# Performance work log

Measured on AMD Instinct MI355X. Metric: run time of the kernel, lower is better.

The kernel has to match this reference:

```python
import jax, jax.numpy as jnp
import numpy as np

HEADS = 8
HEAD_DIM = 64
EPS = 1e-5


def setup_inputs() -> dict:
    key = jax.random.key(0)
    k1, k2, k3 = jax.random.split(key, 3)
    dim, hidden = 512, HEADS * HEAD_DIM
    x = jax.random.normal(k1, (8, dim, 64, 64), dtype=jnp.float32)
    w_qkv = jax.random.normal(k2, (hidden * 3, dim), dtype=jnp.float32) * (dim ** -0.5)
    w_out = jax.random.normal(k3, (dim, hidden), dtype=jnp.float32) * (hidden ** -0.5)
    b_out = jnp.zeros((dim,), dtype=jnp.float32)
    g = jnp.ones((dim,), dtype=jnp.float32)
    return {"x": x, "w_qkv": w_qkv, "w_out": w_out, "b_out": b_out, "g": g}


def reference(x, w_qkv, w_out, b_out, g):
    b, c, h, w = x.shape
    n = h * w
    scale = HEAD_DIM ** -0.5
    xf = x.reshape(b, c, n)  # 1x1 conv == channel matmul
    qkv = jnp.einsum('oc,bcn->bon', w_qkv, xf)
    q, k, v = jnp.split(qkv, 3, axis=1)
    def to_heads(t):
        return t.reshape(b, HEADS, HEAD_DIM, n)
    q, k, v = to_heads(q), to_heads(k), to_heads(v)
    q = jax.nn.softmax(q, axis=-2) * scale   # softmax over head_dim
    k = jax.nn.softmax(k, axis=-1)           # softmax over tokens
    v = v / n
    # context: (B,H,d,d) = k (B,H,d,N) @ v^T (B,H,N,e)
    context = jnp.einsum('bhdn,bhen->bhde', k, v)
    # out: context^T (e,d) @ q (d,N) -> (B,H,e,N)
    out = jnp.einsum('bhde,bhdn->bhen', context, q)
    out = out.reshape(b, HEADS * HEAD_DIM, n)
    y = jnp.einsum('co,bon->bcn', w_out, out) + b_out[None, :, None]
    # channel LayerNorm (mean/var over dim=1, biased var, scale g only)
    mean = jnp.mean(y, axis=1, keepdims=True)
    var = jnp.var(y, axis=1, keepdims=True)
    y = (y - mean) * jax.lax.rsqrt(var + EPS) * g[None, :, None]
    return y.reshape(b, c, h, w)
```

## Files before the change

### kernel.cpp

```cpp
#include <hip/hip_runtime.h>
#include <math.h>

#define BB 8
#define NN 4096
#define CD 512
#define HH 8
#define DD 64
#define OC3 1536
#define NSPLIT 16

typedef _Float16 f16;
typedef _Float16 half8 __attribute__((ext_vector_type(8)));
typedef _Float16 half4v __attribute__((ext_vector_type(4)));
typedef float f32x4 __attribute__((ext_vector_type(4)));

__device__ __forceinline__ void gload_lds16(const void* g, void* l) {
    __builtin_amdgcn_global_load_lds(
        (const __attribute__((address_space(1))) unsigned int*)g,
        (__attribute__((address_space(3))) unsigned int*)l, 16, 0, 0);
}

__global__ __launch_bounds__(256) void split_w_kernel(
    const float* __restrict__ w, f16* __restrict__ wh, f16* __restrict__ wl)
{
    int idx = blockIdx.x * 256 + threadIdx.x;
    float4 v = ((const float4*)w)[idx];
    float a[4] = {v.x, v.y, v.z, v.w};
    half4v h, l;
    #pragma unroll
    for (int i = 0; i < 4; ++i) {
        float s = a[i] * 64.f;
        f16 hh = (f16)s;
        h[i] = hh;
        l[i] = (f16)(s - (float)hh);
    }
    *(half4v*)(&wh[(long)idx * 4]) = h;
    *(half4v*)(&wl[(long)idx * 4]) = l;
}

__global__ __launch_bounds__(256) void split_x_kernel(
    const float* __restrict__ x, f16* __restrict__ xth, f16* __restrict__ xtl)
{
    __shared__ float tile[64][65];
    int b = blockIdx.z;
    int n0 = blockIdx.x * 64, c0 = blockIdx.y * 64;
    const float* xb = x + ((long)b * CD + c0) * NN + n0;
    int t = threadIdx.x;
    int tr = t >> 6, tc = t & 63;
    #pragma unroll
    for (int i = 0; i < 16; ++i)
        tile[tr + i * 4][tc] = xb[(long)(tr + i * 4) * NN + tc];
    __syncthreads();

    int nl = t >> 3, ck = (t & 7) * 8;
    long obase = ((long)b * NN + n0) * CD + c0;
    #pragma unroll
    for (int p = 0; p < 2; ++p) {
        int n = nl + p * 32;
        half8 h, l;
        #pragma unroll
        for (int j = 0; j < 8; ++j) {
            float s = tile[ck + j][n] * 16.f;
            f16 hv = (f16)s;
            h[j] = hv;
            l[j] = (f16)(s - (float)hv);
        }
        *(half8*)(&xth[obase + (long)n * CD + ck]) = h;
        *(half8*)(&xtl[obase + (long)n * CD + ck]) = l;
    }
}

#define AR  16384
#define BUF 65536

#define STAGE(Lb, k0s)  do {                                                   \
    long kb_ = (long)(k0s) * 2;                                                \
    _Pragma("unroll")                                                          \
    for (int c_ = 0; c_ < 2; ++c_) {                                           \
        long rowoff_ = (long)(rb0 + c_ * 16) * 1024;                           \
        long ldsoff_ = (long)(rb0 + c_ * 16) * 64;                             \
        gload_lds16(gA_h + rowoff_ + kb_ + g_lane, (Lb) + 0 * AR + ldsoff_);   \
        gload_lds16(gA_l + rowoff_ + kb_ + g_lane, (Lb) + 1 * AR + ldsoff_);   \
        gload_lds16(gB_h + rowoff_ + kb_ + g_lane, (Lb) + 2 * AR + ldsoff_);   \
        gload_lds16(gB_l + rowoff_ + kb_ + g_lane, (Lb) + 3 * AR + ldsoff_);   \
    } } while (0)

__global__ __launch_bounds__(512, 2) void mfma_gemm_kernel(
    const f16* __restrict__ Ah, const f16* __restrict__ Al, long sA,
    const f16* __restrict__ Bh, const f16* __restrict__ Bl, long sB,
    float* __restrict__ Cp, long sC, int ldC,
    const float* __restrict__ bias, const float* __restrict__ inv_sc,
    float base_sc, int fuseqv)
{
    __shared__ f16 lds[2][4][256 * 32];
    int bz = blockIdx.z;
    int n0 = blockIdx.x * 256, m0 = blockIdx.y * 256;
    int t = threadIdx.x;
    int lane = t & 63, wid = t >> 6;
    int wy = wid >> 2, wx = wid & 3;

    int cl = (lane & 3) ^ ((lane >> 3) & 3);
    long g_lane = (long)(lane >> 2) * 1024 + (long)cl * 16;

    const char* gA_h = (const char*)(Ah + bz * sA) + (long)m0 * 1024;
    const char* gA_l = (const char*)(Al + bz * sA) + (long)m0 * 1024;
    const char* gB_h = (const char*)(Bh + bz * sB) + (long)n0 * 1024;
    const char* gB_l = (const char*)(Bl + bz * sB) + (long)n0 * 1024;

    char* L0 = (char*)&lds[0][0][0];
    int rb0 = wid * 32;

    int cp = (lane >> 4) ^ (((lane & 15) >> 1) & 3);
    long offA = (long)(wy * 128 + (lane & 15)) * 64 + (long)cp * 16;
    long offB = (long)(wx * 64 + (lane & 15)) * 64 + (long)cp * 16;

    f32x4 acc[8][4];
    #pragma unroll
    for (int i = 0; i < 8; ++i)
        #pragma unroll
        for (int j = 0; j < 4; ++j)
            acc[i][j] = (f32x4){0.f, 0.f, 0.f, 0.f};

    STAGE(L0, 0);
    asm volatile("s_waitcnt vmcnt(0)" ::: "memory");
    __syncthreads();

    for (int s = 0; s < 16; ++s) {
        char* Lc = L0 + ((s & 1) ? BUF : 0);
        if (s < 15) {
            char* Ln = L0 + (((s + 1) & 1) ? BUF : 0);
            STAGE(Ln, (s + 1) * 32);
        }

        half8 ah[8], al[8];
        #pragma unroll
        for (int i = 0; i < 8; ++i) {
            ah[i] = *(const half8*)(Lc + 0 * AR + offA + i * 1024);
            al[i] = *(const half8*)(Lc + 1 * AR + offA + i * 1024);
        }
        #pragma unroll
        for (int j = 0; j < 4; ++j) {
            half8 bh = *(const half8*)(Lc + 2 * AR + offB + j * 1024);
            half8 bl = *(const half8*)(Lc + 3 * AR + offB + j * 1024);
            #pragma unroll
            for (int i = 0; i < 8; ++i) {
                acc[i][j] = __builtin_amdgcn_mfma_f32_16x16x32_f16(ah[i], bh, acc[i][j], 0, 0, 0);
                acc[i][j] = __builtin_amdgcn_mfma_f32_16x16x32_f16(ah[i], bl, acc[i][j], 0, 0, 0);
                acc[i][j] = __builtin_amdgcn_mfma_f32_16x16x32_f16(al[i], bh, acc[i][j], 0, 0, 0);
            }
        }

        asm volatile("s_waitcnt vmcnt(0)" ::: "memory");
        __syncthreads();
    }

    int colb = n0 + wx * 64 + (lane & 15);
    int rowb = m0 + wy * 128 + ((lane >> 4) << 2);

    if (fuseqv && m0 < 512) {
        int h0 = (m0 >> 6) + wy * 2;
        f16* qh_b = (f16*)(Cp + (long)bz * sC);
        f16* ql_b = qh_b + (long)CD * NN;
        #pragma unroll
        for (int i = 0; i < 8; ++i)
            #pragma unroll
            for (int j = 0; j < 4; ++j)
                #pragma unroll
                for (int r = 0; r < 4; ++r)
                    acc[i][j][r] *= base_sc;
        #pragma unroll
        for (int j = 0; j < 4; ++j) {
            long nj = colb + j * 16;
            #pragma unroll
            for (int g = 0; g < 2; ++g) {
                float mx = -INFINITY;
                #pragma unroll
                for (int di = 0; di < 4; ++di)
                    #pragma unroll
                    for (int r = 0; r < 4; ++r)
                        mx = fmaxf(mx, acc[g * 4 + di][j][r]);
                mx = fmaxf(mx, __shfl_xor(mx, 16));
                mx = fmaxf(mx, __shfl_xor(mx, 32));
                float sum = 0.f;
                #pragma unroll
                for (int di = 0; di < 4; ++di)
                    #pragma unroll
                    for (int r = 0; r < 4; ++r) {
                        float e = expf(acc[g * 4 + di][j][r] - mx);
                        acc[g * 4 + di][j][r] = e;
                        sum += e;
                    }
                sum += __shfl_xor(sum, 16);
                sum += __shfl_xor(sum, 32);
                float rj = 32.f / sum;
                long off = nj * CD + (h0 + g) * 64 + ((lane >> 4) << 2);
                #pragma unroll
                for (int di = 0; di < 4; ++di) {
                    half4v hh, ll;
                    #pragma unroll
                    for (int r = 0; r < 4; ++r) {
                        float v = acc[g * 4 + di][j][r] * rj;
                        f16 hv = (f16)v;
                        hh[r] = hv;
                        ll[r] = (f16)(v - (float)hv);
                    }
                    *(half4v*)(qh_b + off + di * 16) = hh;
                    *(half4v*)(ql_b + off + di * 16) = ll;
                }
            }
        }
        return;
    }

    if (fuseqv && m0 >= 1024) {
        f16* vhp = (f16*)(Cp + (long)bz * sC + 2L * CD * NN);
        f16* vlp = vhp + (long)CD * NN;
        float vsc = base_sc * 16.f;
        #pragma unroll
        for (int i = 0; i < 8; ++i)
            #pragma unroll
            for (int j = 0; j < 4; ++j)
                #pragma unroll
                for (int r = 0; r < 4; ++r) {
                    long row = rowb + i * 16 + r - 1024;
                    float val = acc[i][j][r] * vsc;
                    f16 hv = (f16)val;
                    vhp[row * NN + colb + j * 16] = hv;
                    vlp[row * NN + colb + j * 16] = (f16)(val - (float)hv);
                }
        return;
    }

    float* outp = Cp + bz * sC;
    float mult = base_sc * (inv_sc ? inv_sc[bz] : 1.f);
    #pragma unroll
    for (int i = 0; i < 8; ++i)
        #pragma unroll
        for (int j = 0; j < 4; ++j)
            #pragma unroll
            for (int r = 0; r < 4; ++r) {
                int row = rowb + i * 16 + r;
                float bb = bias ? bias[row] : 0.f;
                outp[(long)row * ldC + colb + j * 16] = acc[i][j][r] * mult + bb;
            }
}

__global__ __launch_bounds__(256) void softmax_k_kernel(
    const float* __restrict__ qkv, f16* __restrict__ ksp)
{
    int row = blockIdx.x;
    int b = row >> 9;
    int hd = row & (CD - 1);
    const float* base = qkv + ((long)b * OC3 + CD + hd) * NN;
    f16* khb = ksp + (long)b * 2 * CD * NN + (long)hd * NN;
    f16* klb = khb + (long)CD * NN;
    int t = threadIdx.x;

    float v[16];
    #pragma unroll
    for (int i = 0; i < 16; ++i) v[i] = base[t + i * 256];

    __shared__ float red[256];
    float mx = -INFINITY;
    #pragma unroll
    for (int i = 0; i < 16; ++i) mx = fmaxf(mx, v[i]);
    red[t] = mx; __syncthreads();
    for (int off = 128; off > 0; off >>= 1) {
        if (t < off) red[t] = fmaxf(red[t], red[t + off]);
        __syncthreads();
    }
    mx = red[0]; __syncthreads();

    float s = 0.f;
    #pragma unroll
    for (int i = 0; i < 16; ++i) {
        v[i] = expf(v[i] - mx);
        s += v[i];
    }
    red[t] = s; __syncthreads();
    for (int off = 128; off > 0; off >>= 1) {
        if (t < off) red[t] += red[t + off];
        __syncthreads();
    }
    float inv = 4096.f / red[0];

    #pragma unroll
    for (int i = 0; i < 16; ++i) {
        float val = v[i] * inv;
        f16 hv = (f16)val;
        khb[t + i * 256] = hv;
        klb[t + i * 256] = (f16)(val - (float)hv);
    }
}

__global__ __launch_bounds__(256) void ctx_mfma_kernel(
    const f16* __restrict__ ksp, const float* __restrict__ qkv,
    float* __restrict__ ctxp)
{
    __shared__ f16 lds[4][64 * 32];
    int sp = blockIdx.x;
    int bh = blockIdx.y;
    int b = bh >> 3, h = bh & 7;
    int t = threadIdx.x, lane = t & 63, w = t >> 6;

    const char* khg = (const char*)(ksp + (long)b * 2 * CD * NN) + (long)h * 64 * (NN * 2);
    const char* klg = khg + (long)CD * NN * 2;
    const char* vhg = (const char*)(qkv + ((long)b * OC3 + 2L * CD) * NN) + (long)h * 64 * (NN * 2);
    const char* vlg = vhg + (long)CD * NN * 2;
    const char* gw = (w == 0) ? khg : (w == 1) ? klg : (w == 2) ? vhg : vlg;

    int cl = (lane & 3) ^ ((lane >> 3) & 3);
    char* larr = (char*)&lds[0][0] + w * 4096;
    char* L = (char*)&lds[0][0];
    int cp16 = ((lane >> 4) ^ (((lane & 15) >> 1) & 3)) * 16;
    int lr = lane & 15;

    f32x4 acc[4];
    #pragma unroll
    for (int i = 0; i < 4; ++i) acc[i] = (f32x4){0.f, 0.f, 0.f, 0.f};

    for (int ks = 0; ks < 8; ++ks) {
        long kbyte = ((long)sp * 256 + ks * 32) * 2;
        #pragma unroll
        for (int c = 0; c < 4; ++c)
            gload_lds16(gw + (long)(c * 16 + (lane >> 2)) * (NN * 2) + kbyte + (long)cl * 16,
                        larr + c * 1024 + lane * 16);
        asm volatile("s_waitcnt vmcnt(0)" ::: "memory");
        __syncthreads();

        half8 ah[4], al[4], bhf, blf;
        #pragma unroll
        for (int i = 0; i < 4; ++i) {
            ah[i] = *(const half8*)(L + 0 * 4096 + (i * 16 + lr) * 64 + cp16);
            al[i] = *(const half8*)(L + 1 * 4096 + (i * 16 + lr) * 64 + cp16);
        }
        bhf = *(const half8*)(L + 2 * 4096 + (w * 16 + lr) * 64 + cp16);
        blf = *(const half8*)(L + 3 * 4096 + (w * 16 + lr) * 64 + cp16);
        #pragma unroll
        for (int i = 0; i < 4; ++i) {
            acc[i] = __builtin_amdgcn_mfma_f32_16x16x32_f16(ah[i], bhf, acc[i], 0, 0, 0);
            acc[i] = __builtin_amdgcn_mfma_f32_16x16x32_f16(ah[i], blf, acc[i], 0, 0, 0);
            acc[i] = __builtin_amdgcn_mfma_f32_16x16x32_f16(al[i], bhf, acc[i], 0, 0, 0);
        }
        __syncthreads();
    }

    float* op = ctxp + ((long)bh * NSPLIT + sp) * 4096;
    #pragma unroll
    for (int i = 0; i < 4; ++i)
        #pragma unroll
        for (int r = 0; r < 4; ++r)
            op[(i * 16 + (lane >> 4) * 4 + r) * 64 + w * 16 + lr] = acc[i][r];
}

__global__ __launch_bounds__(256) void fold_wout_kernel(
    const float* __restrict__ w_out, const float* __restrict__ ctxp,
    float* __restrict__ Mf)
{
    __shared__ float cl[64][65];
    int bh = blockIdx.x;
    int b = bh >> 3, h = bh & 7;
    int t = threadIdx.x;
    const float* cp = ctxp + (long)bh * NSPLIT * 4096;
    #pragma unroll
    for (int i = 0; i < 16; ++i) {
        int de = t + i * 256;
        double s = 0.0;
        #pragma unroll
        for (int sp = 0; sp < NSPLIT; ++sp)
            s += (double)cp[(long)sp * 4096 + de];
        cl[de >> 6][de & 63] = (float)(s * (1.0 / 268435456.0));
    }
    __syncthreads();

    int d = t & 63, tc = t >> 6;
    for (int ci = 0; ci < 128; ++ci) {
        int c = tc * 128 + ci;
        const float* wr = w_out + (long)c * CD + h * DD;
        float s = 0.f;
        #pragma unroll
        for (int e = 0; e < 64; ++e) s += wr[e] * cl[d][e];
        Mf[((long)b * CD + c) * CD + h * DD + d] = s;
    }
}

__global__ __launch_bounds__(256) void max_m_part_kernel(
    const float* __restrict__ Mf, float* __restrict__ part)
{
    int blk = blockIdx.x;
    int b = blk >> 5, sub = blk & 31;
    const float4* p = (const float4*)(Mf + (long)b * CD * CD) + (long)sub * 2048;
    float mx = 0.f;
    for (int i = threadIdx.x; i < 2048; i += 256) {
        float4 v = p[i];
        mx = fmaxf(mx, fmaxf(fmaxf(fabsf(v.x), fabsf(v.y)),
                             fmaxf(fabsf(v.z), fabsf(v.w))));
    }
    __shared__ float red[256];
    red[threadIdx.x] = mx; __syncthreads();
    for (int off = 128; off > 0; off >>= 1) {
        if (threadIdx.x < off) red[threadIdx.x] = fmaxf(red[threadIdx.x], red[threadIdx.x + off]);
        __syncthreads();
    }
    if (threadIdx.x == 0) part[blk] = red[0];
}

__global__ __launch_bounds__(64) void max_m_final_kernel(
    const float* __restrict__ part, float* __restrict__ scl)
{
    int b = threadIdx.x;
    if (b < 8) {
        float m = 0.f;
        #pragma unroll
        for (int i = 0; i < 32; ++i) m = fmaxf(m, part[b * 32 + i]);
        int e = (m > 1e-30f) ? ilogbf(m) : 0;
        scl[b] = ldexpf(1.f, 10 - e);
        scl[8 + b] = ldexpf(1.f, e - 10);
    }
}

__global__ __launch_bounds__(256) void split_m_kernel(
    const float* __restrict__ Mf, const float* __restrict__ scl,
    f16* __restrict__ mh, f16* __restrict__ ml)
{
    int idx = blockIdx.x * 256 + threadIdx.x;
    float s = scl[idx >> 16];
    float4 v = ((const float4*)Mf)[idx];
    float a[4] = {v.x, v.y, v.z, v.w};
    half4v h, l;
    #pragma unroll
    for (int i = 0; i < 4; ++i) {
        float tval = a[i] * s;
        f16 hv = (f16)tval;
        h[i] = hv;
        l[i] = (f16)(tval - (float)hv);
    }
    *(half4v*)(&mh[(long)idx * 4]) = h;
    *(half4v*)(&ml[(long)idx * 4]) = l;
}

__global__ __launch_bounds__(256) void layernorm_kernel(
    const float* __restrict__ qkv, const float* __restrict__ g,
    float* __restrict__ out)
{
    int t = threadIdx.x;
    int tn = t & 31, cy = t >> 5;
    long col = (long)blockIdx.x * 32 + tn;
    int n = (int)(col & (NN - 1));
    int b = (int)(col >> 12);
    const float* base = qkv + (long)b * OC3 * NN + (long)CD * NN + n;

    float v[64];
    double s = 0.0, ss = 0.0;
    #pragma unroll
    for (int i = 0; i < 64; ++i) {
        v[i] = base[(long)(cy * 64 + i) * NN];
        s += (double)v[i];
        ss += (double)v[i] * (double)v[i];
    }

    __shared__ double rs[8][32], rss[8][32];
    rs[cy][tn] = s; rss[cy][tn] = ss;
    __syncthreads();
    __shared__ float mb[32], ib[32];
    if (cy == 0) {
        double S = 0.0, SS = 0.0;
        #pragma unroll
        for (int j = 0; j < 8; ++j) { S += rs[j][tn]; SS += rss[j][tn]; }
        double mean = S * (1.0 / CD);
        double var = SS * (1.0 / CD) - mean * mean;
        mb[tn] = (float)mean;
        ib[tn] = (float)(1.0 / sqrt(var + 1e-5));
    }
    __syncthreads();
    float m = mb[tn], iv = ib[tn];

    float* oc = out + (long)b * CD * NN + n;
    #pragma unroll
    for (int i = 0; i < 64; ++i)
        oc[(long)(cy * 64 + i) * NN] = (v[i] - m) * iv * g[cy * 64 + i];
}

extern "C" void kernel_launch(void* const* d_in, const int* in_sizes, int n_in,
                              void* d_out, int out_size, void* d_ws, size_t ws_size,
                              hipStream_t stream)
{
    const float* x     = (const float*)d_in[0];
    const float* w_qkv = (const float*)d_in[1];
    const float* w_out = (const float*)d_in[2];
    const float* b_out = (const float*)d_in[3];
    const float* g     = (const float*)d_in[4];
    float* out = (float*)d_out;

    float* ws   = (float*)d_ws;
    float* qkv  = ws;
    float* ctxp = qkv + (long)BB * OC3 * NN;
    f16*   mh   = (f16*)(ctxp + (long)BB * HH * NSPLIT * DD * DD);
    f16*   ml   = mh + (long)BB * CD * CD;
    f16*   wh   = (f16*)(ml + (long)BB * CD * CD);
    f16*   wl   = wh + (long)OC3 * CD;
    float* scl  = (float*)(wl + (long)OC3 * CD);
    float* part = scl + 16;

    f16* xth = (f16*)d_out;
    f16* xtl = xth + (long)BB * NN * CD;
    f16* ksp = (f16*)d_out;
    float* Mf = (float*)d_out;

    split_w_kernel<<<(OC3 * CD / 4) / 256, 256, 0, stream>>>(w_qkv, wh, wl);
    split_x_kernel<<<dim3(NN / 64, CD / 64, BB), 256, 0, stream>>>(x, xth, xtl);

    mfma_gemm_kernel<<<dim3(NN / 256, OC3 / 256, BB), 512, 0, stream>>>(
        wh, wl, 0L, xth, xtl, (long)NN * CD,
        qkv, (long)OC3 * NN, NN, nullptr, nullptr, 1.0f / 1024.0f, 1);

    softmax_k_kernel<<<BB * CD, 256, 0, stream>>>(qkv, ksp);

    ctx_mfma_kernel<<<dim3(NSPLIT, BB * HH), 256, 0, stream>>>(ksp, qkv, ctxp);

    fold_wout_kernel<<<BB * HH, 256, 0, stream>>>(w_out, ctxp, Mf);
    max_m_part_kernel<<<256, 256, 0, stream>>>(Mf, part);
    max_m_final_kernel<<<1, 64, 0, stream>>>(part, scl);
    split_m_kernel<<<(BB * CD * CD / 4) / 256, 256, 0, stream>>>(Mf, scl, mh, ml);

    mfma_gemm_kernel<<<dim3(NN / 256, CD / 256, BB), 512, 0, stream>>>(
        mh, ml, (long)CD * CD,
        (const f16*)qkv, (const f16*)qkv + (long)CD * NN, (long)OC3 * NN * 2,
        qkv + (long)CD * NN, (long)OC3 * NN, NN, b_out, scl + 8, 1.0f / 256.0f,
        0);

    layernorm_kernel<<<(BB * NN) / 32, 256, 0, stream>>>(qkv, g, out);
}
```

Measured before the change: 423.4 us.

## Fuse K softmax into context MFMA kernel and add 128-tile output GEMM

The K softmax no longer writes a normalized f16 hi/lo copy of K. A row-stat kernel now stores only the per-row max and inverse sum. The context kernel loads raw fp32 K, applies exp and scale, and splits it into hi/lo halves in registers before the MFMAs, which removes a full write and re-read of K. The final output GEMM moves to a new 128x128-tile kernel with 256 threads, which launches more blocks for the small M=512 case. The cost is recomputing exp inside the context kernel and reading fp32 K at twice the byte width.

```diff
diff --git a/kernel.cpp b/kernel.cpp
--- a/kernel.cpp
+++ b/kernel.cpp
@@ -88,9 +88,7 @@
 __global__ __launch_bounds__(512, 2) void mfma_gemm_kernel(
     const f16* __restrict__ Ah, const f16* __restrict__ Al, long sA,
     const f16* __restrict__ Bh, const f16* __restrict__ Bl, long sB,
-    float* __restrict__ Cp, long sC, int ldC,
-    const float* __restrict__ bias, const float* __restrict__ inv_sc,
-    float base_sc, int fuseqv)
+    float* __restrict__ Cp, long sC, int ldC, float base_sc)
 {
     __shared__ f16 lds[2][4][256 * 32];
     int bz = blockIdx.z;
@@ -157,7 +155,7 @@
     int colb = n0 + wx * 64 + (lane & 15);
     int rowb = m0 + wy * 128 + ((lane >> 4) << 2);
 
-    if (fuseqv && m0 < 512) {
+    if (m0 < 512) {
         int h0 = (m0 >> 6) + wy * 2;
         f16* qh_b = (f16*)(Cp + (long)bz * sC);
         f16* ql_b = qh_b + (long)CD * NN;
@@ -212,7 +210,7 @@
         return;
     }
 
-    if (fuseqv && m0 >= 1024) {
+    if (m0 >= 1024) {
         f16* vhp = (f16*)(Cp + (long)bz * sC + 2L * CD * NN);
         f16* vlp = vhp + (long)CD * NN;
         float vsc = base_sc * 16.f;
@@ -232,9 +230,106 @@
     }
 
     float* outp = Cp + bz * sC;
+    #pragma unroll
+    for (int i = 0; i < 8; ++i)
+        #pragma unroll
+        for (int j = 0; j < 4; ++j)
+            #pragma unroll
+            for (int r = 0; r < 4; ++r) {
+                int row = rowb + i * 16 + r;
+                outp[(long)row * ldC + colb + j * 16] = acc[i][j][r] * base_sc;
+            }
+}
+
+#define AR2  8192
+#define BUF2 32768
+
+#define STAGE2(Lb, k0s)  do {                                                  \
+    long kb_ = (long)(k0s) * 2;                                                \
+    _Pragma("unroll")                                                          \
+    for (int c_ = 0; c_ < 2; ++c_) {                                           \
+        long rowoff_ = (long)(rb0 + c_ * 16) * 1024;                           \
+        long ldsoff_ = (long)(rb0 + c_ * 16) * 64;                             \
+        gload_lds16(gA_h + rowoff_ + kb_ + g_lane, (Lb) + 0 * AR2 + ldsoff_);  \
+        gload_lds16(gA_l + rowoff_ + kb_ + g_lane, (Lb) + 1 * AR2 + ldsoff_);  \
+        gload_lds16(gB_h + rowoff_ + kb_ + g_lane, (Lb) + 2 * AR2 + ldsoff_);  \
+        gload_lds16(gB_l + rowoff_ + kb_ + g_lane, (Lb) + 3 * AR2 + ldsoff_);  \
+    } } while (0)
+
+__global__ __launch_bounds__(256) void mfma_gemm128_kernel(
+    const f16* __restrict__ Ah, const f16* __restrict__ Al, long sA,
+    const f16* __restrict__ Bh, const f16* __restrict__ Bl, long sB,
+    float* __restrict__ Cp, long sC, int ldC,
+    const float* __restrict__ bias, const float* __restrict__ inv_sc,
+    float base_sc)
+{
+    __shared__ f16 lds[2][4][128 * 32];
+    int bz = blockIdx.z;
+    int n0 = blockIdx.x * 128, m0 = blockIdx.y * 128;
+    int t = threadIdx.x;
+    int lane = t & 63, wid = t >> 6;
+    int wy = wid >> 1, wx = wid & 1;
+
+    int cl = (lane & 3) ^ ((lane >> 3) & 3);
+    long g_lane = (long)(lane >> 2) * 1024 + (long)cl * 16;
+
+    const char* gA_h = (const char*)(Ah + bz * sA) + (long)m0 * 1024;
+    const char* gA_l = (const char*)(Al + bz * sA) + (long)m0 * 1024;
+    const char* gB_h = (const char*)(Bh + bz * sB) + (long)n0 * 1024;
+    const char* gB_l = (const char*)(Bl + bz * sB) + (long)n0 * 1024;
+
+    char* L0 = (char*)&lds[0][0][0];
+    int rb0 = wid * 32;
+
+    int cp = (lane >> 4) ^ (((lane & 15) >> 1) & 3);
+    long offA = (long)(wy * 64 + (lane & 15)) * 64 + (long)cp * 16;
+    long offB = (long)(wx * 64 + (lane & 15)) * 64 + (long)cp * 16;
+
+    f32x4 acc[4][4];
+    #pragma unroll
+    for (int i = 0; i < 4; ++i)
+        #pragma unroll
+        for (int j = 0; j < 4; ++j)
+            acc[i][j] = (f32x4){0.f, 0.f, 0.f, 0.f};
+
+    STAGE2(L0, 0);
+    asm volatile("s_waitcnt vmcnt(0)" ::: "memory");
+    __syncthreads();
+
+    for (int s = 0; s < 16; ++s) {
+        char* Lc = L0 + ((s & 1) ? BUF2 : 0);
+        if (s < 15) {
+            char* Ln = L0 + (((s + 1) & 1) ? BUF2 : 0);
+            STAGE2(Ln, (s + 1) * 32);
+        }
+
+        half8 ah[4], al[4], bh[4], bl[4];
+        #pragma unroll
+        for (int i = 0; i < 4; ++i) {
+            ah[i] = *(const half8*)(Lc + 0 * AR2 + offA + i * 1024);
+            al[i] = *(const half8*)(Lc + 1 * AR2 + offA + i * 1024);
+            bh[i] = *(const half8*)(Lc + 2 * AR2 + offB + i * 1024);
+            bl[i] = *(const half8*)(Lc + 3 * AR2 + offB + i * 1024);
+        }
+        #pragma unroll
+        for (int i = 0; i < 4; ++i)
+            #pragma unroll
+            for (int j = 0; j < 4; ++j) {
+                acc[i][j] = __builtin_amdgcn_mfma_f32_16x16x32_f16(ah[i], bh[j], acc[i][j], 0, 0, 0);
+                acc[i][j] = __builtin_amdgcn_mfma_f32_16x16x32_f16(ah[i], bl[j], acc[i][j], 0, 0, 0);
+                acc[i][j] = __builtin_amdgcn_mfma_f32_16x16x32_f16(al[i], bh[j], acc[i][j], 0, 0, 0);
+            }
+
+        asm volatile("s_waitcnt vmcnt(0)" ::: "memory");
+        __syncthreads();
+    }
+
+    int colb = n0 + wx * 64 + (lane & 15);
+    int rowb = m0 + wy * 64 + ((lane >> 4) << 2);
+    float* outp = Cp + bz * sC;
     float mult = base_sc * (inv_sc ? inv_sc[bz] : 1.f);
     #pragma unroll
-    for (int i = 0; i < 8; ++i)
+    for (int i = 0; i < 4; ++i)
         #pragma unroll
         for (int j = 0; j < 4; ++j)
             #pragma unroll
@@ -245,15 +340,14 @@
             }
 }
 
-__global__ __launch_bounds__(256) void softmax_k_kernel(
-    const float* __restrict__ qkv, f16* __restrict__ ksp)
+__global__ __launch_bounds__(256) void k_rowstat_kernel(
+    const float* __restrict__ qkv, float* __restrict__ statmx,
+    float* __restrict__ statinv)
 {
     int row = blockIdx.x;
     int b = row >> 9;
     int hd = row & (CD - 1);
     const float* base = qkv + ((long)b * OC3 + CD + hd) * NN;
-    f16* khb = ksp + (long)b * 2 * CD * NN + (long)hd * NN;
-    f16* klb = khb + (long)CD * NN;
     int t = threadIdx.x;
 
     float v[16];
@@ -282,60 +376,86 @@
         if (t < off) red[t] += red[t + off];
         __syncthreads();
     }
-    float inv = 4096.f / red[0];
-
-    #pragma unroll
-    for (int i = 0; i < 16; ++i) {
-        float val = v[i] * inv;
-        f16 hv = (f16)val;
-        khb[t + i * 256] = hv;
-        klb[t + i * 256] = (f16)(val - (float)hv);
+    if (t == 0) {
+        statmx[row] = mx;
+        statinv[row] = 4096.f / red[0];
     }
 }
 
 __global__ __launch_bounds__(256) void ctx_mfma_kernel(
-    const f16* __restrict__ ksp, const float* __restrict__ qkv,
-    float* __restrict__ ctxp)
-{
-    __shared__ f16 lds[4][64 * 32];
+    const float* __restrict__ qkv, const float* __restrict__ statmx,
+    const float* __restrict__ statinv, float* __restrict__ ctxp)
+{
+    __shared__ char lds[16384];
     int sp = blockIdx.x;
     int bh = blockIdx.y;
     int b = bh >> 3, h = bh & 7;
     int t = threadIdx.x, lane = t & 63, w = t >> 6;
 
-    const char* khg = (const char*)(ksp + (long)b * 2 * CD * NN) + (long)h * 64 * (NN * 2);
-    const char* klg = khg + (long)CD * NN * 2;
+    const char* kg = (const char*)(qkv + ((long)b * OC3 + CD + (long)h * 64) * NN);
     const char* vhg = (const char*)(qkv + ((long)b * OC3 + 2L * CD) * NN) + (long)h * 64 * (NN * 2);
     const char* vlg = vhg + (long)CD * NN * 2;
-    const char* gw = (w == 0) ? khg : (w == 1) ? klg : (w == 2) ? vhg : vlg;
+
+    int lr = lane & 15, hi = lane >> 4;
+    float mx[4], inv[4];
+    #pragma unroll
+    for (int i = 0; i < 4; ++i) {
+        int ridx = b * CD + h * 64 + i * 16 + lr;
+        mx[i] = statmx[ridx];
+        inv[i] = statinv[ridx];
+    }
 
     int cl = (lane & 3) ^ ((lane >> 3) & 3);
-    char* larr = (char*)&lds[0][0] + w * 4096;
-    char* L = (char*)&lds[0][0];
-    int cp16 = ((lane >> 4) ^ (((lane & 15) >> 1) & 3)) * 16;
-    int lr = lane & 15;
+    int cp16 = (hi ^ ((lr >> 1) & 3)) * 16;
+
+    int ksrow = (lane >> 3);
+    int ksc = lane & 7;
 
     f32x4 acc[4];
     #pragma unroll
     for (int i = 0; i < 4; ++i) acc[i] = (f32x4){0.f, 0.f, 0.f, 0.f};
 
+    int s7 = lr & 7;
+
     for (int ks = 0; ks < 8; ++ks) {
-        long kbyte = ((long)sp * 256 + ks * 32) * 2;
-        #pragma unroll
-        for (int c = 0; c < 4; ++c)
-            gload_lds16(gw + (long)(c * 16 + (lane >> 2)) * (NN * 2) + kbyte + (long)cl * 16,
-                        larr + c * 1024 + lane * 16);
+        int n0 = sp * 256 + ks * 32;
+        if (w < 2) {
+            #pragma unroll
+            for (int it2 = 0; it2 < 4; ++it2) {
+                int it = w * 4 + it2;
+                int r = it * 8 + ksrow;
+                gload_lds16(kg + (long)r * (NN * 4) + (long)n0 * 4 + ((ksc ^ (r & 7)) << 4),
+                            lds + it * 1024 + lane * 16);
+            }
+        } else {
+            const char* gv = (w == 2) ? vhg : vlg;
+            char* lv = lds + 8192 + (w - 2) * 4096;
+            #pragma unroll
+            for (int c2 = 0; c2 < 4; ++c2)
+                gload_lds16(gv + (long)(c2 * 16 + (lane >> 2)) * (NN * 2) + (long)n0 * 2 + (long)cl * 16,
+                            lv + c2 * 1024 + lane * 16);
+        }
         asm volatile("s_waitcnt vmcnt(0)" ::: "memory");
         __syncthreads();
 
-        half8 ah[4], al[4], bhf, blf;
+        half8 ah[4], al[4];
         #pragma unroll
         for (int i = 0; i < 4; ++i) {
-            ah[i] = *(const half8*)(L + 0 * 4096 + (i * 16 + lr) * 64 + cp16);
-            al[i] = *(const half8*)(L + 1 * 4096 + (i * 16 + lr) * 64 + cp16);
-        }
-        bhf = *(const half8*)(L + 2 * 4096 + (w * 16 + lr) * 64 + cp16);
-        blf = *(const half8*)(L + 3 * 4096 + (w * 16 + lr) * 64 + cp16);
+            int row = i * 16 + lr;
+            const char* rb = lds + row * 128;
+            f32x4 a0 = *(const f32x4*)(rb + (((2 * hi) ^ s7) << 4));
+            f32x4 a1 = *(const f32x4*)(rb + (((2 * hi + 1) ^ s7) << 4));
+            #pragma unroll
+            for (int j = 0; j < 8; ++j) {
+                float kv = (j < 4) ? a0[j] : a1[j - 4];
+                float e = expf(kv - mx[i]) * inv[i];
+                f16 hv = (f16)e;
+                ah[i][j] = hv;
+                al[i][j] = (f16)(e - (float)hv);
+            }
+        }
+        half8 bhf = *(const half8*)(lds + 8192 + (w * 16 + lr) * 64 + cp16);
+        half8 blf = *(const half8*)(lds + 12288 + (w * 16 + lr) * 64 + cp16);
         #pragma unroll
         for (int i = 0; i < 4; ++i) {
             acc[i] = __builtin_amdgcn_mfma_f32_16x16x32_f16(ah[i], bhf, acc[i], 0, 0, 0);
@@ -350,7 +470,7 @@
     for (int i = 0; i < 4; ++i)
         #pragma unroll
         for (int r = 0; r < 4; ++r)
-            op[(i * 16 + (lane >> 4) * 4 + r) * 64 + w * 16 + lr] = acc[i][r];
+            op[(i * 16 + hi * 4 + r) * 64 + w * 16 + lr] = acc[i][r];
 }
 
 __global__ __launch_bounds__(256) void fold_wout_kernel(
@@ -501,10 +621,11 @@
     f16*   wl   = wh + (long)OC3 * CD;
     float* scl  = (float*)(wl + (long)OC3 * CD);
     float* part = scl + 16;
+    float* statmx = part + 256;
+    float* statinv = statmx + BB * CD;
 
     f16* xth = (f16*)d_out;
     f16* xtl = xth + (long)BB * NN * CD;
-    f16* ksp = (f16*)d_out;
     float* Mf = (float*)d_out;
 
     split_w_kernel<<<(OC3 * CD / 4) / 256, 256, 0, stream>>>(w_qkv, wh, wl);
@@ -512,22 +633,22 @@
 
     mfma_gemm_kernel<<<dim3(NN / 256, OC3 / 256, BB), 512, 0, stream>>>(
         wh, wl, 0L, xth, xtl, (long)NN * CD,
-        qkv, (long)OC3 * NN, NN, nullptr, nullptr, 1.0f / 1024.0f, 1);
-
-    softmax_k_kernel<<<BB * CD, 256, 0, stream>>>(qkv, ksp);
-
-    ctx_mfma_kernel<<<dim3(NSPLIT, BB * HH), 256, 0, stream>>>(ksp, qkv, ctxp);
+        qkv, (long)OC3 * NN, NN, 1.0f / 1024.0f);
+
+    k_rowstat_kernel<<<BB * CD, 256, 0, stream>>>(qkv, statmx, statinv);
+
+    ctx_mfma_kernel<<<dim3(NSPLIT, BB * HH), 256, 0, stream>>>(
+        qkv, statmx, statinv, ctxp);
 
     fold_wout_kernel<<<BB * HH, 256, 0, stream>>>(w_out, ctxp, Mf);
     max_m_part_kernel<<<256, 256, 0, stream>>>(Mf, part);
     max_m_final_kernel<<<1, 64, 0, stream>>>(part, scl);
     split_m_kernel<<<(BB * CD * CD / 4) / 256, 256, 0, stream>>>(Mf, scl, mh, ml);
 
-    mfma_gemm_kernel<<<dim3(NN / 256, CD / 256, BB), 512, 0, stream>>>(
+    mfma_gemm128_kernel<<<dim3(NN / 128, CD / 128, BB), 256, 0, stream>>>(
         mh, ml, (long)CD * CD,
         (const f16*)qkv, (const f16*)qkv + (long)CD * NN, (long)OC3 * NN * 2,
-        qkv + (long)CD * NN, (long)OC3 * NN, NN, b_out, scl + 8, 1.0f / 256.0f,
-        0);
+        qkv + (long)CD * NN, (long)OC3 * NN, NN, b_out, scl + 8, 1.0f / 256.0f);
 
     layernorm_kernel<<<(BB * NN) / 32, 256, 0, stream>>>(qkv, g, out);
 }
```

Result: slower. 434.7 us (+2.7%).
